# Kernel tuning notes

Hardware: AMD Instinct MI355X
Metric: run time of the kernel (lower is better)

## Reference

```python
import jax, jax.numpy as jnp
import numpy as np

B, SQ, SK, D, H, F = 8, 512, 1024, 1024, 16, 4096
DK = D // H
NEG_INF = -jnp.inf


def _linear(x, w, b):
    return x @ w + b


def _mha(q, k, v, wq, bq, wk, bk, wv, bv, wo, bo, causal, kv_mask):
    # q: [B,Sq,D], k/v: [B,Sk,D]
    b, sq, d = q.shape
    sk = k.shape[1]
    Q = _linear(q, wq, bq).reshape(b, sq, H, DK).transpose(0, 2, 1, 3)  # [B,H,Sq,dk]
    K = _linear(k, wk, bk).reshape(b, sk, H, DK).transpose(0, 2, 1, 3)
    V = _linear(v, wv, bv).reshape(b, sk, H, DK).transpose(0, 2, 1, 3)
    S = jnp.einsum('bhqd,bhkd->bhqk', Q, K) / jnp.sqrt(jnp.asarray(DK, Q.dtype))
    if kv_mask is not None:
        S = jnp.where(kv_mask[:, None, None, :] == 0, NEG_INF, S)
    if causal:
        tri = jnp.tril(jnp.ones((sq, sk), dtype=bool))
        S = jnp.where(tri, S, NEG_INF)
    A = jax.nn.softmax(S, axis=-1)  # dropout p=0 -> identity
    x = jnp.einsum('bhqk,bhkd->bhqd', A, V).transpose(0, 2, 1, 3).reshape(b, sq, d)
    return _linear(x, wo, bo), A


def _ln(x, g, beta, eps=1e-5):
    mu = jnp.mean(x, axis=-1, keepdims=True)
    var = jnp.mean(jnp.square(x - mu), axis=-1, keepdims=True)
    return (x - mu) * jax.lax.rsqrt(var + eps) * g + beta


def setup_inputs() -> dict:
    key = jax.random.key(0)
    ks = jax.random.split(key, 32)
    s = 0.02
    inp = {
        'x': jax.random.normal(ks[0], (B, SQ, D), jnp.float32),
        'enc_o': jax.random.normal(ks[1], (B, SK, D), jnp.float32),
        'enc_mask': jax.random.randint(ks[2], (B, SK), 0, 2, jnp.int32),
    }
    i = 3
    for pfx in ('a1', 'a2'):
        for nm in ('wq', 'wk', 'wv', 'wo'):
            inp[f'{pfx}_{nm}'] = jax.random.normal(ks[i], (D, D), jnp.float32) * s; i += 1
            inp[f'{pfx}_{nm[1:] and "b" + nm[1:]}'] = jnp.zeros((D,), jnp.float32)
    inp['ff_w1'] = jax.random.normal(ks[i], (D, F), jnp.float32) * s; i += 1
    inp['ff_b1'] = jnp.zeros((F,), jnp.float32)
    inp['ff_w2'] = jax.random.normal(ks[i], (F, D), jnp.float32) * s; i += 1
    inp['ff_b2'] = jnp.zeros((D,), jnp.float32)
    for n in ('ln1', 'ln2', 'ln3'):
        inp[f'{n}_g'] = jnp.ones((D,), jnp.float32)
        inp[f'{n}_b'] = jnp.zeros((D,), jnp.float32)
    return inp


def reference(x, enc_o, enc_mask,
              a1_wq, a1_bq, a1_wk, a1_bk, a1_wv, a1_bv, a1_wo, a1_bo,
              a2_wq, a2_bq, a2_wk, a2_bk, a2_wv, a2_bv, a2_wo, a2_bo,
              ff_w1, ff_b1, ff_w2, ff_b2,
              ln1_g, ln1_b, ln2_g, ln2_b, ln3_g, ln3_b):
    res, _ = _mha(x, x, x, a1_wq, a1_bq, a1_wk, a1_bk, a1_wv, a1_bv, a1_wo, a1_bo,
                  causal=True, kv_mask=None)
    x = _ln(x + res, ln1_g, ln1_b)
    res, attn = _mha(x, enc_o, enc_o, a2_wq, a2_bq, a2_wk, a2_bk, a2_wv, a2_bv, a2_wo, a2_bo,
                     causal=False, kv_mask=enc_mask)
    x = _ln(x + res, ln2_g, ln2_b)
    res = _linear(jax.nn.relu(_linear(x, ff_w1, ff_b1)), ff_w2, ff_b2)
    x = _ln(x + res, ln3_g, ln3_b)
    return (x, attn)
```

## Files before the change

kernel.cpp:

```cpp
#include <hip/hip_runtime.h>
#include <hip/hip_bf16.h>


using bf16 = __hip_bfloat16;
typedef __attribute__((ext_vector_type(8))) short short8;
typedef __attribute__((ext_vector_type(4))) float f32x4;

#define DEVINL __device__ __forceinline__

DEVINL unsigned short bf16bits(float f) {
  __hip_bfloat16 h = __float2bfloat16(f);
  return *reinterpret_cast<unsigned short*>(&h);
}
DEVINL float bits2f(unsigned short u) {
  return __uint_as_float(((unsigned int)u) << 16);
}
DEVINL float tofloat(float f) { return f; }
DEVINL float tofloat(bf16 h) { return __bfloat162float(h); }

#define GLD16(gp, lp) __builtin_amdgcn_global_load_lds( \
    (__attribute__((address_space(1))) const void*)(gp), \
    (__attribute__((address_space(3))) void*)(lp), 16, 0, 0)

struct GemmP {
  const bf16* A; const bf16* Bt; void* C;
  const float* bias; const int* kmask;
  float scale;
  int M, N, K, lda, ldb, ldc;
  long sAb, sAh, sBb, sBh, sCb, sCh;
};

enum { EPI_BIAS_BF16 = 0, EPI_CAUSAL_BF16, EPI_KMASK_F32, EPI_NONE_BF16,
       EPI_BIAS_F32, EPI_BIAS_RELU_BF16, EPI_PART_F32 };

template<int EPI>
__global__ __launch_bounds__(256)
void gemm_k(GemmP p) {
  __shared__ bf16 As[128 * 32];
  __shared__ bf16 Bs[128 * 32];
  const int t = threadIdx.x;
  const int lane = t & 63;
  const int w = t >> 6;
  const int z = blockIdx.z;
  const int zb = z >> 4, zh = z & 15;
  const int m0 = blockIdx.y * 128, n0 = blockIdx.x * 128;

  const bf16* Ab = p.A + (long)zb * p.sAb + (long)zh * p.sAh;
  const bf16* Bb = p.Bt + (long)zb * p.sBb + (long)zh * p.sBh;
  const int fl = lane & 15, fq = lane >> 4;
  const int wm = (w >> 1) * 64, wn = (w & 1) * 64;

  f32x4 acc[4][4];
#pragma unroll
  for (int i = 0; i < 4; ++i)
#pragma unroll
    for (int j = 0; j < 4; ++j) acc[i][j] = (f32x4){0.f, 0.f, 0.f, 0.f};

  const int sr = t >> 2;
  const int sc = (t & 3) * 8;
  char* ldsA = (char*)As + w * 1024;
  char* ldsB = (char*)Bs + w * 1024;

  int brow0 = n0 + sr;      if (brow0 > p.N - 1) brow0 = p.N - 1;
  int brow1 = n0 + sr + 64; if (brow1 > p.N - 1) brow1 = p.N - 1;

  for (int k0 = 0; k0 < p.K; k0 += 32) {
    GLD16(Ab + (long)(m0 + sr) * p.lda + k0 + sc, ldsA);
    GLD16(Ab + (long)(m0 + sr + 64) * p.lda + k0 + sc, ldsA + 4096);
    GLD16(Bb + (long)brow0 * p.ldb + k0 + sc, ldsB);
    GLD16(Bb + (long)brow1 * p.ldb + k0 + sc, ldsB + 4096);
    __syncthreads();

    short8 af[4], bfv[4];
#pragma unroll
    for (int i = 0; i < 4; ++i)
      af[i] = *(const short8*)(As + (wm + i * 16 + fl) * 32 + fq * 8);
#pragma unroll
    for (int j = 0; j < 4; ++j)
      bfv[j] = *(const short8*)(Bs + (wn + j * 16 + fl) * 32 + fq * 8);
#pragma unroll
    for (int i = 0; i < 4; ++i)
#pragma unroll
      for (int j = 0; j < 4; ++j)
        acc[i][j] = __builtin_amdgcn_mfma_f32_16x16x32_bf16(af[i], bfv[j], acc[i][j], 0, 0, 0);
    __syncthreads();
  }

  const float NEGINF = -__builtin_inff();
  const long cbase = (long)zb * p.sCb + (long)zh * p.sCh;
#pragma unroll
  for (int i = 0; i < 4; ++i) {
#pragma unroll
    for (int j = 0; j < 4; ++j) {
#pragma unroll
      for (int r = 0; r < 4; ++r) {
        int row = m0 + wm + i * 16 + fq * 4 + r;
        int col = n0 + wn + j * 16 + fl;
        if (col < p.N) {
          float v = acc[i][j][r];
          if (EPI == EPI_BIAS_BF16 || EPI == EPI_BIAS_F32 || EPI == EPI_BIAS_RELU_BF16)
            v += p.bias[col];
          if (EPI == EPI_BIAS_RELU_BF16) v = v > 0.f ? v : 0.f;
          if (EPI == EPI_CAUSAL_BF16) { v *= p.scale; if (col > row) v = NEGINF; }
          if (EPI == EPI_KMASK_F32)   { v *= p.scale; if (p.kmask[zb * 1024 + col] == 0) v = NEGINF; }
          long off = cbase + (long)row * p.ldc + col;
          if (EPI == EPI_KMASK_F32 || EPI == EPI_BIAS_F32 || EPI == EPI_PART_F32)
            ((float*)p.C)[off] = v;
          else ((bf16*)p.C)[off] = __float2bfloat16(v);
        }
      }
    }
  }
}

struct AttnP {
  const bf16 *Q, *K, *Vt;
  float* Pout; bf16* O;
  const int* kmask;
  int ldq, ldk, ldv;
  long sQb, sQh, sKb, sKh, sVb, sVh, sPb, sPh, sOb, sOh;
};

template<int SK, bool CAUSAL, bool WRITE_P>
__global__ __launch_bounds__(512)
void attn_fused_k(AttnP p) {
  constexpr int TKMAX = SK / 64;
  __shared__ bf16 S[64 * SK];
  __shared__ bf16 ring[3 * 4096];
  const int t = threadIdx.x;
  const int lane = t & 63;
  const int w = t >> 6;
  const int fl = lane & 15, fq = lane >> 4;
  const int qh = w >> 2;
  const int wc = w & 3;
  const int zb = blockIdx.z >> 4, zh = blockIdx.z & 15;
  const int q0 = blockIdx.y * 64;
  const float NEGINF = -__builtin_inff();

  const bf16* Qb = p.Q + (long)zb * p.sQb + (long)zh * p.sQh;
  const bf16* Kb = p.K + (long)zb * p.sKb + (long)zh * p.sKh;
  const bf16* Vb = p.Vt + (long)zb * p.sVb + (long)zh * p.sVh;

  const int Tk = CAUSAL ? (q0 >> 6) + 1 : TKMAX;

  short8 af[2][2];
#pragma unroll
  for (int i = 0; i < 2; ++i)
#pragma unroll
    for (int kk = 0; kk < 2; ++kk)
      af[i][kk] = *(const short8*)(Qb + (long)(q0 + qh * 32 + i * 16 + fl) * p.ldq + kk * 32 + fq * 8);

  int kmv[CAUSAL ? 1 : TKMAX];
  if (!CAUSAL) {
#pragma unroll
    for (int kt = 0; kt < TKMAX; ++kt)
      kmv[kt] = p.kmask[zb * 1024 + kt * 64 + wc * 16 + fl];
  }

  const int so = t * 16;
  const int srow = so >> 7;
  const int scb = (so & 127) ^ ((srow & 7) << 4);
  auto stage = [&](const bf16* mb, int ld, int roff, int coff, int buf) {
    GLD16(mb + (long)(roff + srow) * ld + coff + (scb >> 1),
          (char*)ring + buf * 8192 + so);
  };

  stage(Kb, p.ldk, 0, 0, 0);
  if (Tk > 1) stage(Kb, p.ldk, 64, 0, 1);
  for (int kt = 0; kt < Tk; ++kt) {
    if (kt + 1 < Tk) asm volatile("s_waitcnt vmcnt(1)" ::: "memory");
    else             asm volatile("s_waitcnt vmcnt(0)" ::: "memory");
    __builtin_amdgcn_s_barrier();
    if (kt + 2 < Tk) stage(Kb, p.ldk, (kt + 2) * 64, 0, (kt + 2) % 3);

    const char* kb = (const char*)ring + (kt % 3) * 8192;
    const int krow = wc * 16 + fl;
    short8 bfv[2];
#pragma unroll
    for (int kk = 0; kk < 2; ++kk)
      bfv[kk] = *(const short8*)(kb + ((krow * 128 + kk * 64 + fq * 16) ^ ((krow & 7) << 4)));
    f32x4 acc[2] = {(f32x4){0.f,0.f,0.f,0.f}, (f32x4){0.f,0.f,0.f,0.f}};
#pragma unroll
    for (int kk = 0; kk < 2; ++kk) {
      acc[0] = __builtin_amdgcn_mfma_f32_16x16x32_bf16(af[0][kk], bfv[kk], acc[0], 0, 0, 0);
      acc[1] = __builtin_amdgcn_mfma_f32_16x16x32_bf16(af[1][kk], bfv[kk], acc[1], 0, 0, 0);
    }
    const int col = kt * 64 + wc * 16 + fl;
    const bool mok = CAUSAL || (kmv[CAUSAL ? 0 : kt] != 0);
#pragma unroll
    for (int i = 0; i < 2; ++i) {
#pragma unroll
      for (int r = 0; r < 4; ++r) {
        int row = qh * 32 + i * 16 + fq * 4 + r;
        float v = acc[i][r] * 0.125f;
        if (CAUSAL) { if (col > q0 + row) v = NEGINF; }
        else if (!mok) v = NEGINF;
        int b = ((row * SK + col) * 2) ^ ((row & 7) << 4);
        *(bf16*)((char*)S + b) = __float2bfloat16(v);
      }
    }
  }
  asm volatile("s_waitcnt lgkmcnt(0)" ::: "memory");
  __builtin_amdgcn_s_barrier();

  const int Tv = Tk;
  stage(Vb, p.ldv, 0, 0, 0);
  if (Tv > 1) stage(Vb, p.ldv, 0, 64, 1);

  float* Pf = WRITE_P ? (p.Pout + (long)zb * p.sPb + (long)zh * p.sPh) : nullptr;
  constexpr int NC = SK / 512;
  const int lim = Tk * 64;
  for (int rr = 0; rr < 8; ++rr) {
    const int row = w * 8 + rr;
    const int swz = (row & 7) << 4;
    float fv[NC][8];
#pragma unroll
    for (int c = 0; c < NC; ++c) {
      const int col = c * 512 + lane * 8;
      if (!CAUSAL || col < lim) {
        short8 sv = *(const short8*)((char*)S + (((row * SK + col) * 2) ^ swz));
#pragma unroll
        for (int j = 0; j < 8; ++j) fv[c][j] = bits2f((unsigned short)sv[j]);
      } else {
#pragma unroll
        for (int j = 0; j < 8; ++j) fv[c][j] = NEGINF;
      }
    }
    float mx = fv[0][0];
#pragma unroll
    for (int c = 0; c < NC; ++c)
#pragma unroll
      for (int j = 0; j < 8; ++j) mx = fmaxf(mx, fv[c][j]);
    for (int off = 32; off; off >>= 1) mx = fmaxf(mx, __shfl_xor(mx, off, 64));
    float s = 0.f;
#pragma unroll
    for (int c = 0; c < NC; ++c)
#pragma unroll
      for (int j = 0; j < 8; ++j) { fv[c][j] = expf(fv[c][j] - mx); s += fv[c][j]; }
    for (int off = 32; off; off >>= 1) s += __shfl_xor(s, off, 64);
    const float inv = 1.f / s;
#pragma unroll
    for (int c = 0; c < NC; ++c) {
      const int col = c * 512 + lane * 8;
      if (!CAUSAL || col < lim) {
        short8 o;
#pragma unroll
        for (int j = 0; j < 8; ++j) o[j] = (short)bf16bits(fv[c][j] * inv);
        *(short8*)((char*)S + (((row * SK + col) * 2) ^ swz)) = o;
        if (WRITE_P) {
          float* pp = Pf + (long)(q0 + row) * SK + col;
          f32x4 o0, o1;
#pragma unroll
          for (int j = 0; j < 4; ++j) { o0[j] = fv[c][j] * inv; o1[j] = fv[c][4 + j] * inv; }
          *(f32x4*)pp = o0;
          *(f32x4*)(pp + 4) = o1;
        }
      }
    }
  }
  asm volatile("s_waitcnt lgkmcnt(0)" ::: "memory");
  __builtin_amdgcn_s_barrier();

  f32x4 ao[2] = {(f32x4){0.f,0.f,0.f,0.f}, (f32x4){0.f,0.f,0.f,0.f}};
  for (int vt = 0; vt < Tv; ++vt) {
    if (vt + 1 < Tv) asm volatile("s_waitcnt vmcnt(1)" ::: "memory");
    else             asm volatile("s_waitcnt vmcnt(0)" ::: "memory");
    __builtin_amdgcn_s_barrier();
    if (vt + 2 < Tv) stage(Vb, p.ldv, 0, (vt + 2) * 64, (vt + 2) % 3);

    const char* vbuf = (const char*)ring + (vt % 3) * 8192;
    const int vrow = wc * 16 + fl;
    short8 bv[2];
#pragma unroll
    for (int kk = 0; kk < 2; ++kk)
      bv[kk] = *(const short8*)(vbuf + ((vrow * 128 + kk * 64 + fq * 16) ^ ((vrow & 7) << 4)));
#pragma unroll
    for (int i = 0; i < 2; ++i) {
      const int row = qh * 32 + i * 16 + fl;
#pragma unroll
      for (int kk = 0; kk < 2; ++kk) {
        const int col = vt * 64 + kk * 32 + fq * 8;
        short8 pa = *(const short8*)((char*)S + (((row * SK + col) * 2) ^ ((row & 7) << 4)));
        ao[i] = __builtin_amdgcn_mfma_f32_16x16x32_bf16(pa, bv[kk], ao[i], 0, 0, 0);
      }
    }
  }

  bf16* Ob_ = p.O + (long)zb * p.sOb + (long)zh * p.sOh;
#pragma unroll
  for (int i = 0; i < 2; ++i)
#pragma unroll
    for (int r = 0; r < 4; ++r) {
      int row = q0 + qh * 32 + i * 16 + fq * 4 + r;
      Ob_[(long)row * 1024 + wc * 16 + fl] = __float2bfloat16(ao[i][r]);
    }
}

__global__ __launch_bounds__(256)
void ln_k(const float* __restrict__ x, const float* __restrict__ r,
          const float* __restrict__ g, const float* __restrict__ bt,
          float* __restrict__ outf, bf16* __restrict__ outb) {
  const int lane = threadIdx.x & 63;
  const long row = (long)blockIdx.x * 4 + (threadIdx.x >> 6);
  const float* px = x + row * 1024;
  const float* pr = r + row * 1024;
  float4 v[4];
  float s = 0.f;
#pragma unroll
  for (int c = 0; c < 4; ++c) {
    float4 a = *(const float4*)(px + c * 256 + lane * 4);
    float4 b = *(const float4*)(pr + c * 256 + lane * 4);
    v[c].x = a.x + b.x; v[c].y = a.y + b.y; v[c].z = a.z + b.z; v[c].w = a.w + b.w;
    s += v[c].x + v[c].y + v[c].z + v[c].w;
  }
  for (int off = 32; off; off >>= 1) s += __shfl_xor(s, off, 64);
  float mu = s * (1.f / 1024.f);
  float q = 0.f;
#pragma unroll
  for (int c = 0; c < 4; ++c) {
    float dx = v[c].x - mu, dy = v[c].y - mu, dz = v[c].z - mu, dw = v[c].w - mu;
    q += dx * dx + dy * dy + dz * dz + dw * dw;
  }
  for (int off = 32; off; off >>= 1) q += __shfl_xor(q, off, 64);
  float rs = rsqrtf(q * (1.f / 1024.f) + 1e-5f);
#pragma unroll
  for (int c = 0; c < 4; ++c) {
    int col = c * 256 + lane * 4;
    float4 gg = *(const float4*)(g + col);
    float4 bb = *(const float4*)(bt + col);
    float4 o;
    o.x = (v[c].x - mu) * rs * gg.x + bb.x;
    o.y = (v[c].y - mu) * rs * gg.y + bb.y;
    o.z = (v[c].z - mu) * rs * gg.z + bb.z;
    o.w = (v[c].w - mu) * rs * gg.w + bb.w;
    *(float4*)(outf + row * 1024 + col) = o;
    if (outb) {
      uint2 pk;
      pk.x = bf16bits(o.x) | ((unsigned)bf16bits(o.y) << 16);
      pk.y = bf16bits(o.z) | ((unsigned)bf16bits(o.w) << 16);
      *(uint2*)(outb + row * 1024 + col) = pk;
    }
  }
}

template<typename TI>
__global__ __launch_bounds__(256)
void transpose_k(const TI* __restrict__ in, bf16* __restrict__ out,
                 int R, int C, int ldi, int ldo,
                 long sInb, long sInh, long sOutb, long sOuth) {
  __shared__ float tile[32][33];
  const int zb = blockIdx.z >> 4, zh = blockIdx.z & 15;
  const TI* pin = in + (long)zb * sInb + (long)zh * sInh;
  bf16* pout = out + (long)zb * sOutb + (long)zh * sOuth;
  const int c0 = blockIdx.x * 32, r0 = blockIdx.y * 32;
  const int tx = threadIdx.x & 31, ty = threadIdx.x >> 5;
#pragma unroll
  for (int i = 0; i < 32; i += 8)
    tile[ty + i][tx] = tofloat(pin[(long)(r0 + ty + i) * ldi + c0 + tx]);
  __syncthreads();
#pragma unroll
  for (int i = 0; i < 32; i += 8)
    pout[(long)(c0 + ty + i) * ldo + r0 + tx] = __float2bfloat16(tile[tx][ty + i]);
}

__global__ __launch_bounds__(256) void cvt_k(const float* __restrict__ in,
                                             bf16* __restrict__ out, long n4) {
  long i = (long)blockIdx.x * 256 + threadIdx.x;
  if (i < n4) {
    float4 v = *(const float4*)(in + i * 4);
    uint2 pk;
    pk.x = bf16bits(v.x) | ((unsigned)bf16bits(v.y) << 16);
    pk.y = bf16bits(v.z) | ((unsigned)bf16bits(v.w) << 16);
    *(uint2*)(out + i * 4) = pk;
  }
}

__global__ __launch_bounds__(256)
void concatb_k(float* dst, const float* a, const float* b, const float* c,
               int n, int total) {
  int i = blockIdx.x * 256 + threadIdx.x;
  if (i >= total) return;
  float v = (i < n) ? a[i] : (i < 2 * n ? b[i - n] : c[i - 2 * n]);
  dst[i] = v;
}

__global__ __launch_bounds__(256)
void reduce4_k(const float* __restrict__ part, const float* __restrict__ bias,
               float* __restrict__ out) {
  long i = ((long)blockIdx.x * 256 + threadIdx.x) * 4;
  float4 a = *(const float4*)(part + i);
  float4 b = *(const float4*)(part + 4194304 + i);
  float4 c = *(const float4*)(part + 2 * 4194304 + i);
  float4 d = *(const float4*)(part + 3 * 4194304 + i);
  float4 bi = *(const float4*)(bias + (int)(i & 1023));
  float4 o;
  o.x = a.x + b.x + c.x + d.x + bi.x;
  o.y = a.y + b.y + c.y + d.y + bi.y;
  o.z = a.z + b.z + c.z + d.z + bi.z;
  o.w = a.w + b.w + c.w + d.w + bi.w;
  *(float4*)(out + i) = o;
}

static inline GemmP mkp(const void* A, const bf16* Bt, void* C,
                        const float* bias, const int* km, float sc,
                        int M, int N, int K, int lda, int ldb, int ldc,
                        long sAb, long sAh, long sBb, long sBh, long sCb, long sCh) {
  GemmP p;
  p.A = (const bf16*)A; p.Bt = Bt; p.C = C; p.bias = bias; p.kmask = km; p.scale = sc;
  p.M = M; p.N = N; p.K = K; p.lda = lda; p.ldb = ldb; p.ldc = ldc;
  p.sAb = sAb; p.sAh = sAh; p.sBb = sBb; p.sBh = sBh; p.sCb = sCb; p.sCh = sCh;
  return p;
}

extern "C" void kernel_launch(void* const* d_in, const int* in_sizes, int n_in,
                              void* d_out, int out_size, void* d_ws, size_t ws_size,
                              hipStream_t stream) {
  const float* x        = (const float*)d_in[0];
  const float* enc_o    = (const float*)d_in[1];
  const int*   enc_mask = (const int*)d_in[2];
  const float* a1_wq = (const float*)d_in[3];  const float* a1_bq = (const float*)d_in[4];
  const float* a1_wk = (const float*)d_in[5];  const float* a1_bk = (const float*)d_in[6];
  const float* a1_wv = (const float*)d_in[7];  const float* a1_bv = (const float*)d_in[8];
  const float* a1_wo = (const float*)d_in[9];  const float* a1_bo = (const float*)d_in[10];
  const float* a2_wq = (const float*)d_in[11]; const float* a2_bq = (const float*)d_in[12];
  const float* a2_wk = (const float*)d_in[13]; const float* a2_bk = (const float*)d_in[14];
  const float* a2_wv = (const float*)d_in[15]; const float* a2_bv = (const float*)d_in[16];
  const float* a2_wo = (const float*)d_in[17]; const float* a2_bo = (const float*)d_in[18];
  const float* ff_w1 = (const float*)d_in[19]; const float* ff_b1 = (const float*)d_in[20];
  const float* ff_w2 = (const float*)d_in[21]; const float* ff_b2 = (const float*)d_in[22];
  const float* ln1_g = (const float*)d_in[23]; const float* ln1_b = (const float*)d_in[24];
  const float* ln2_g = (const float*)d_in[25]; const float* ln2_b = (const float*)d_in[26];
  const float* ln3_g = (const float*)d_in[27]; const float* ln3_b = (const float*)d_in[28];

  const size_t MB = 1u << 20;
  const long M1 = 1048576;
  char* w = (char*)d_ws;
  bf16*  xb   = (bf16*)(w + 0);
  bf16*  encb = (bf16*)(w + 8 * MB);
  float* x1f  = (float*)(w + 24 * MB);
  float* x2f  = (float*)(w + 40 * MB);
  bf16*  xcb  = (bf16*)(w + 56 * MB);
  bf16*  wT   = (bf16*)(w + 64 * MB);
  float* bqkv = (float*)(w + 96 * MB);
  float* bkv  = (float*)(w + 96 * MB + 16384);
  bf16*  QKV  = (bf16*)(w + 104 * MB);
  bf16*  KVc  = (bf16*)(w + 128 * MB);
  bf16*  Vt   = (bf16*)(w + 160 * MB);
  bf16*  Ob   = (bf16*)(w + 176 * MB);
  float* res  = (float*)(w + 184 * MB);
  float* part = (float*)(w + 200 * MB);
  bf16*  Asf  = (bf16*)(w + 264 * MB);

  float* out_x = (float*)d_out;
  float* attn  = (float*)d_out + 4194304;

  const dim3 blk(256);
  const dim3 blk5(512);

  cvt_k<<<4096, blk, 0, stream>>>(x, xb, 1048576);
  cvt_k<<<8192, blk, 0, stream>>>(enc_o, encb, 2097152);
  {
    dim3 tg(32, 32, 1);
    transpose_k<float><<<tg, blk, 0, stream>>>(a1_wq, wT + 0 * M1, 1024, 1024, 1024, 1024, 0,0,0,0);
    transpose_k<float><<<tg, blk, 0, stream>>>(a1_wk, wT + 1 * M1, 1024, 1024, 1024, 1024, 0,0,0,0);
    transpose_k<float><<<tg, blk, 0, stream>>>(a1_wv, wT + 2 * M1, 1024, 1024, 1024, 1024, 0,0,0,0);
    transpose_k<float><<<tg, blk, 0, stream>>>(a1_wo, wT + 3 * M1, 1024, 1024, 1024, 1024, 0,0,0,0);
    transpose_k<float><<<tg, blk, 0, stream>>>(a2_wq, wT + 4 * M1, 1024, 1024, 1024, 1024, 0,0,0,0);
    transpose_k<float><<<tg, blk, 0, stream>>>(a2_wk, wT + 5 * M1, 1024, 1024, 1024, 1024, 0,0,0,0);
    transpose_k<float><<<tg, blk, 0, stream>>>(a2_wv, wT + 6 * M1, 1024, 1024, 1024, 1024, 0,0,0,0);
    transpose_k<float><<<tg, blk, 0, stream>>>(a2_wo, wT + 7 * M1, 1024, 1024, 1024, 1024, 0,0,0,0);
    transpose_k<float><<<dim3(128, 32, 1), blk, 0, stream>>>(ff_w1, wT + 8 * M1, 1024, 4096, 4096, 1024, 0,0,0,0);
    transpose_k<float><<<dim3(32, 128, 1), blk, 0, stream>>>(ff_w2, wT + 12 * M1, 4096, 1024, 1024, 4096, 0,0,0,0);
  }
  concatb_k<<<12, blk, 0, stream>>>(bqkv, a1_bq, a1_bk, a1_bv, 1024, 3072);
  concatb_k<<<8, blk, 0, stream>>>(bkv, a2_bk, a2_bv, a2_bv, 1024, 2048);

  gemm_k<EPI_BIAS_BF16><<<dim3(24, 32, 1), blk, 0, stream>>>(
      mkp(xb, wT, QKV, bqkv, nullptr, 0.f, 4096, 3072, 1024, 1024, 1024, 3072, 0,0,0,0,0,0));
  bf16* Qs = QKV;
  bf16* Ks = QKV + 1024;
  bf16* Vs = QKV + 2048;

  transpose_k<bf16><<<dim3(2, 16, 128), blk, 0, stream>>>(
      Vs, Vt, 512, 64, 3072, 512, 1572864, 64, 524288, 32768);

  {
    AttnP ap;
    ap.Q = Qs; ap.K = Ks; ap.Vt = Vt; ap.Pout = nullptr; ap.O = Ob; ap.kmask = nullptr;
    ap.ldq = 3072; ap.ldk = 3072; ap.ldv = 512;
    ap.sQb = 1572864; ap.sQh = 64; ap.sKb = 1572864; ap.sKh = 64;
    ap.sVb = 524288;  ap.sVh = 32768; ap.sPb = 0; ap.sPh = 0;
    ap.sOb = 524288;  ap.sOh = 64;
    attn_fused_k<512, true, false><<<dim3(1, 8, 128), blk5, 0, stream>>>(ap);
  }

  gemm_k<EPI_BIAS_F32><<<dim3(8, 32, 1), blk, 0, stream>>>(
      mkp(Ob, wT + 3 * M1, res, a1_bo, nullptr, 0.f, 4096, 1024, 1024, 1024, 1024, 1024, 0,0,0,0,0,0));

  ln_k<<<1024, blk, 0, stream>>>(x, res, ln1_g, ln1_b, x1f, xcb);

  gemm_k<EPI_BIAS_BF16><<<dim3(8, 32, 1), blk, 0, stream>>>(
      mkp(xcb, wT + 4 * M1, QKV, a2_bq, nullptr, 0.f, 4096, 1024, 1024, 1024, 1024, 1024, 0,0,0,0,0,0));
  gemm_k<EPI_BIAS_BF16><<<dim3(16, 64, 1), blk, 0, stream>>>(
      mkp(encb, wT + 5 * M1, KVc, bkv, nullptr, 0.f, 8192, 2048, 1024, 1024, 1024, 2048, 0,0,0,0,0,0));
  bf16* Qc = QKV;
  bf16* Kc = KVc;
  bf16* Vc = KVc + 1024;

  transpose_k<bf16><<<dim3(2, 32, 128), blk, 0, stream>>>(
      Vc, Vt, 1024, 64, 2048, 1024, 2097152, 64, 1048576, 65536);

  {
    AttnP ap;
    ap.Q = Qc; ap.K = Kc; ap.Vt = Vt; ap.Pout = attn; ap.O = Ob; ap.kmask = enc_mask;
    ap.ldq = 1024; ap.ldk = 2048; ap.ldv = 1024;
    ap.sQb = 524288;  ap.sQh = 64; ap.sKb = 2097152; ap.sKh = 64;
    ap.sVb = 1048576; ap.sVh = 65536; ap.sPb = 8388608; ap.sPh = 524288;
    ap.sOb = 524288;  ap.sOh = 64;
    attn_fused_k<1024, false, true><<<dim3(1, 8, 128), blk5, 0, stream>>>(ap);
  }

  gemm_k<EPI_BIAS_F32><<<dim3(8, 32, 1), blk, 0, stream>>>(
      mkp(Ob, wT + 7 * M1, res, a2_bo, nullptr, 0.f, 4096, 1024, 1024, 1024, 1024, 1024, 0,0,0,0,0,0));

  ln_k<<<1024, blk, 0, stream>>>(x1f, res, ln2_g, ln2_b, x2f, xcb);

  gemm_k<EPI_BIAS_RELU_BF16><<<dim3(32, 32, 1), blk, 0, stream>>>(
      mkp(xcb, wT + 8 * M1, Asf, ff_b1, nullptr, 0.f, 4096, 4096, 1024, 1024, 1024, 4096, 0,0,0,0,0,0));
  gemm_k<EPI_PART_F32><<<dim3(8, 32, 4), blk, 0, stream>>>(
      mkp(Asf, wT + 12 * M1, part, nullptr, nullptr, 0.f, 4096, 1024, 1024, 4096, 4096, 1024,
          0, 1024, 0, 1024, 0, 4194304));
  reduce4_k<<<4096, blk, 0, stream>>>(part, ff_b2, res);

  ln_k<<<1024, blk, 0, stream>>>(x2f, res, ln3_g, ln3_b, out_x, nullptr);
}
```

Baseline: 1.044 ms.

## Merge prep kernels, batch projection GEMMs, split-K out-proj with LN-fused reduction

```diff
diff --git a/kernel.cpp b/kernel.cpp
--- a/kernel.cpp
+++ b/kernel.cpp
@@ -34,16 +34,14 @@
        EPI_BIAS_F32, EPI_BIAS_RELU_BF16, EPI_PART_F32 };
 
 template<int EPI>
-__global__ __launch_bounds__(256)
-void gemm_k(GemmP p) {
+DEVINL void gemm_body(const GemmP& p, int bx, int by, int bz) {
   __shared__ bf16 As[128 * 32];
   __shared__ bf16 Bs[128 * 32];
   const int t = threadIdx.x;
   const int lane = t & 63;
   const int w = t >> 6;
-  const int z = blockIdx.z;
-  const int zb = z >> 4, zh = z & 15;
-  const int m0 = blockIdx.y * 128, n0 = blockIdx.x * 128;
+  const int zb = bz >> 4, zh = bz & 15;
+  const int m0 = by * 128, n0 = bx * 128;
 
   const bf16* Ab = p.A + (long)zb * p.sAb + (long)zh * p.sAh;
   const bf16* Bb = p.Bt + (long)zb * p.sBb + (long)zh * p.sBh;
@@ -113,6 +111,20 @@
   }
 }
 
+template<int EPI>
+__global__ __launch_bounds__(256)
+void gemm_k(GemmP p) {
+  gemm_body<EPI>(p, blockIdx.x, blockIdx.y, blockIdx.z);
+}
+
+struct Gemm2P { GemmP a, b; int nA, axw, bxw; };
+__global__ __launch_bounds__(256)
+void gemm2_k(Gemm2P q) {
+  const int b = blockIdx.x;
+  if (b < q.nA) gemm_body<EPI_BIAS_BF16>(q.a, b % q.axw, b / q.axw, 0);
+  else { const int c = b - q.nA; gemm_body<EPI_BIAS_BF16>(q.b, c % q.bxw, c / q.bxw, 0); }
+}
+
 struct AttnP {
   const bf16 *Q, *K, *Vt;
   float* Pout; bf16* O;
@@ -296,21 +308,28 @@
     }
 }
 
+template<int NP>
 __global__ __launch_bounds__(256)
-void ln_k(const float* __restrict__ x, const float* __restrict__ r,
-          const float* __restrict__ g, const float* __restrict__ bt,
-          float* __restrict__ outf, bf16* __restrict__ outb) {
+void ln_fuse_k(const float* __restrict__ x, const float* __restrict__ part, long pstride,
+               const float* __restrict__ pb,
+               const float* __restrict__ g, const float* __restrict__ bt,
+               float* __restrict__ outf, bf16* __restrict__ outb) {
   const int lane = threadIdx.x & 63;
   const long row = (long)blockIdx.x * 4 + (threadIdx.x >> 6);
   const float* px = x + row * 1024;
-  const float* pr = r + row * 1024;
   float4 v[4];
   float s = 0.f;
 #pragma unroll
   for (int c = 0; c < 4; ++c) {
-    float4 a = *(const float4*)(px + c * 256 + lane * 4);
-    float4 b = *(const float4*)(pr + c * 256 + lane * 4);
-    v[c].x = a.x + b.x; v[c].y = a.y + b.y; v[c].z = a.z + b.z; v[c].w = a.w + b.w;
+    const int col = c * 256 + lane * 4;
+    float4 a = *(const float4*)(px + col);
+    float4 bb = *(const float4*)(pb + col);
+    v[c].x = a.x + bb.x; v[c].y = a.y + bb.y; v[c].z = a.z + bb.z; v[c].w = a.w + bb.w;
+#pragma unroll
+    for (int sl = 0; sl < NP; ++sl) {
+      float4 pp = *(const float4*)(part + sl * pstride + row * 1024 + col);
+      v[c].x += pp.x; v[c].y += pp.y; v[c].z += pp.z; v[c].w += pp.w;
+    }
     s += v[c].x + v[c].y + v[c].z + v[c].w;
   }
   for (int off = 32; off; off >>= 1) s += __shfl_xor(s, off, 64);
@@ -344,16 +363,9 @@
 }
 
 template<typename TI>
-__global__ __launch_bounds__(256)
-void transpose_k(const TI* __restrict__ in, bf16* __restrict__ out,
-                 int R, int C, int ldi, int ldo,
-                 long sInb, long sInh, long sOutb, long sOuth) {
-  __shared__ float tile[32][33];
-  const int zb = blockIdx.z >> 4, zh = blockIdx.z & 15;
-  const TI* pin = in + (long)zb * sInb + (long)zh * sInh;
-  bf16* pout = out + (long)zb * sOutb + (long)zh * sOuth;
-  const int c0 = blockIdx.x * 32, r0 = blockIdx.y * 32;
-  const int tx = threadIdx.x & 31, ty = threadIdx.x >> 5;
+DEVINL void tr_body(const TI* __restrict__ pin, bf16* __restrict__ pout,
+                    int ldi, int ldo, int c0, int r0, int t, float tile[32][33]) {
+  const int tx = t & 31, ty = t >> 5;
 #pragma unroll
   for (int i = 0; i < 32; i += 8)
     tile[ty + i][tx] = tofloat(pin[(long)(r0 + ty + i) * ldi + c0 + tx]);
@@ -363,42 +375,66 @@
     pout[(long)(c0 + ty + i) * ldo + r0 + tx] = __float2bfloat16(tile[tx][ty + i]);
 }
 
-__global__ __launch_bounds__(256) void cvt_k(const float* __restrict__ in,
-                                             bf16* __restrict__ out, long n4) {
-  long i = (long)blockIdx.x * 256 + threadIdx.x;
-  if (i < n4) {
-    float4 v = *(const float4*)(in + i * 4);
+struct PrepP {
+  const float *x, *enc;
+  const float* wsrc[10];
+  const float *b0, *b1, *b2, *b4, *b5;
+  bf16 *xb, *encb, *wT;
+  float *bqkv, *bkv;
+};
+__global__ __launch_bounds__(256)
+void prep_k(PrepP p) {
+  __shared__ float tile[32][33];
+  const int b = blockIdx.x, t = threadIdx.x;
+  if (b < 12288) {
+    const float* src = (b < 4096) ? p.x : p.enc;
+    bf16* dst = (b < 4096) ? p.xb : p.encb;
+    long i = (long)(b < 4096 ? b : b - 4096) * 256 + t;
+    float4 v = *(const float4*)(src + i * 4);
     uint2 pk;
     pk.x = bf16bits(v.x) | ((unsigned)bf16bits(v.y) << 16);
     pk.y = bf16bits(v.z) | ((unsigned)bf16bits(v.w) << 16);
-    *(uint2*)(out + i * 4) = pk;
-  }
-}
-
+    *(uint2*)(dst + i * 4) = pk;
+  } else if (b < 20480) {
+    int l = b - 12288; int wdx = l >> 10; l &= 1023;
+    tr_body<float>(p.wsrc[wdx], p.wT + (long)wdx * 1048576, 1024, 1024,
+                   (l & 31) * 32, (l >> 5) * 32, t, tile);
+  } else if (b < 24576) {
+    int l = b - 20480;
+    tr_body<float>(p.wsrc[8], p.wT + 8l * 1048576, 4096, 1024,
+                   (l & 127) * 32, (l >> 7) * 32, t, tile);
+  } else if (b < 28672) {
+    int l = b - 24576;
+    tr_body<float>(p.wsrc[9], p.wT + 12l * 1048576, 1024, 4096,
+                   (l % 32) * 32, (l / 32) * 32, t, tile);
+  } else if (b < 28684) {
+    int i = (b - 28672) * 256 + t;
+    p.bqkv[i] = (i < 1024) ? p.b0[i] : (i < 2048 ? p.b1[i - 1024] : p.b2[i - 2048]);
+  } else {
+    int i = (b - 28684) * 256 + t;
+    p.bkv[i] = (i < 1024) ? p.b4[i] : p.b5[i - 1024];
+  }
+}
+
+struct Vt2P { const bf16 *vs, *vc; bf16 *vts, *vtc; };
 __global__ __launch_bounds__(256)
-void concatb_k(float* dst, const float* a, const float* b, const float* c,
-               int n, int total) {
-  int i = blockIdx.x * 256 + threadIdx.x;
-  if (i >= total) return;
-  float v = (i < n) ? a[i] : (i < 2 * n ? b[i - n] : c[i - 2 * n]);
-  dst[i] = v;
-}
-
-__global__ __launch_bounds__(256)
-void reduce4_k(const float* __restrict__ part, const float* __restrict__ bias,
-               float* __restrict__ out) {
-  long i = ((long)blockIdx.x * 256 + threadIdx.x) * 4;
-  float4 a = *(const float4*)(part + i);
-  float4 b = *(const float4*)(part + 4194304 + i);
-  float4 c = *(const float4*)(part + 2 * 4194304 + i);
-  float4 d = *(const float4*)(part + 3 * 4194304 + i);
-  float4 bi = *(const float4*)(bias + (int)(i & 1023));
-  float4 o;
-  o.x = a.x + b.x + c.x + d.x + bi.x;
-  o.y = a.y + b.y + c.y + d.y + bi.y;
-  o.z = a.z + b.z + c.z + d.z + bi.z;
-  o.w = a.w + b.w + c.w + d.w + bi.w;
-  *(float4*)(out + i) = o;
+void vt2_k(Vt2P p) {
+  __shared__ float tile[32][33];
+  const int b = blockIdx.x, t = threadIdx.x;
+  if (b < 4096) {
+    int z = b >> 5, l = b & 31;
+    int zb = z >> 4, zh = z & 15;
+    tr_body<bf16>(p.vs + (long)zb * 1572864 + zh * 64,
+                  p.vts + (long)zb * 524288 + zh * 32768,
+                  3072, 512, (l & 1) * 32, (l >> 1) * 32, t, tile);
+  } else {
+    int c = b - 4096;
+    int z = c >> 6, l = c & 63;
+    int zb = z >> 4, zh = z & 15;
+    tr_body<bf16>(p.vc + (long)zb * 2097152 + zh * 64,
+                  p.vtc + (long)zb * 1048576 + zh * 65536,
+                  2048, 1024, (l & 1) * 32, (l >> 1) * 32, t, tile);
+  }
 }
 
 static inline GemmP mkp(const void* A, const bf16* Bt, void* C,
@@ -445,11 +481,11 @@
   float* bkv  = (float*)(w + 96 * MB + 16384);
   bf16*  QKV  = (bf16*)(w + 104 * MB);
   bf16*  KVc  = (bf16*)(w + 128 * MB);
-  bf16*  Vt   = (bf16*)(w + 160 * MB);
+  bf16*  VtS  = (bf16*)(w + 160 * MB);
   bf16*  Ob   = (bf16*)(w + 176 * MB);
-  float* res  = (float*)(w + 184 * MB);
   float* part = (float*)(w + 200 * MB);
   bf16*  Asf  = (bf16*)(w + 264 * MB);
+  bf16*  VtC  = (bf16*)(w + 332 * MB);
 
   float* out_x = (float*)d_out;
   float* attn  = (float*)d_out + 4194304;
@@ -457,36 +493,38 @@
   const dim3 blk(256);
   const dim3 blk5(512);
 
-  cvt_k<<<4096, blk, 0, stream>>>(x, xb, 1048576);
-  cvt_k<<<8192, blk, 0, stream>>>(enc_o, encb, 2097152);
   {
-    dim3 tg(32, 32, 1);
-    transpose_k<float><<<tg, blk, 0, stream>>>(a1_wq, wT + 0 * M1, 1024, 1024, 1024, 1024, 0,0,0,0);
-    transpose_k<float><<<tg, blk, 0, stream>>>(a1_wk, wT + 1 * M1, 1024, 1024, 1024, 1024, 0,0,0,0);
-    transpose_k<float><<<tg, blk, 0, stream>>>(a1_wv, wT + 2 * M1, 1024, 1024, 1024, 1024, 0,0,0,0);
-    transpose_k<float><<<tg, blk, 0, stream>>>(a1_wo, wT + 3 * M1, 1024, 1024, 1024, 1024, 0,0,0,0);
-    transpose_k<float><<<tg, blk, 0, stream>>>(a2_wq, wT + 4 * M1, 1024, 1024, 1024, 1024, 0,0,0,0);
-    transpose_k<float><<<tg, blk, 0, stream>>>(a2_wk, wT + 5 * M1, 1024, 1024, 1024, 1024, 0,0,0,0);
-    transpose_k<float><<<tg, blk, 0, stream>>>(a2_wv, wT + 6 * M1, 1024, 1024, 1024, 1024, 0,0,0,0);
-    transpose_k<float><<<tg, blk, 0, stream>>>(a2_wo, wT + 7 * M1, 1024, 1024, 1024, 1024, 0,0,0,0);
-    transpose_k<float><<<dim3(128, 32, 1), blk, 0, stream>>>(ff_w1, wT + 8 * M1, 1024, 4096, 4096, 1024, 0,0,0,0);
-    transpose_k<float><<<dim3(32, 128, 1), blk, 0, stream>>>(ff_w2, wT + 12 * M1, 4096, 1024, 1024, 4096, 0,0,0,0);
-  }
-  concatb_k<<<12, blk, 0, stream>>>(bqkv, a1_bq, a1_bk, a1_bv, 1024, 3072);
-  concatb_k<<<8, blk, 0, stream>>>(bkv, a2_bk, a2_bv, a2_bv, 1024, 2048);
-
-  gemm_k<EPI_BIAS_BF16><<<dim3(24, 32, 1), blk, 0, stream>>>(
-      mkp(xb, wT, QKV, bqkv, nullptr, 0.f, 4096, 3072, 1024, 1024, 1024, 3072, 0,0,0,0,0,0));
+    PrepP pp;
+    pp.x = x; pp.enc = enc_o;
+    pp.wsrc[0] = a1_wq; pp.wsrc[1] = a1_wk; pp.wsrc[2] = a1_wv; pp.wsrc[3] = a1_wo;
+    pp.wsrc[4] = a2_wq; pp.wsrc[5] = a2_wk; pp.wsrc[6] = a2_wv; pp.wsrc[7] = a2_wo;
+    pp.wsrc[8] = ff_w1; pp.wsrc[9] = ff_w2;
+    pp.b0 = a1_bq; pp.b1 = a1_bk; pp.b2 = a1_bv; pp.b4 = a2_bk; pp.b5 = a2_bv;
+    pp.xb = xb; pp.encb = encb; pp.wT = wT; pp.bqkv = bqkv; pp.bkv = bkv;
+    prep_k<<<28692, blk, 0, stream>>>(pp);
+  }
+
+  {
+    Gemm2P q;
+    q.a = mkp(xb, wT, QKV, bqkv, nullptr, 0.f, 4096, 3072, 1024, 1024, 1024, 3072, 0,0,0,0,0,0);
+    q.b = mkp(encb, wT + 5 * M1, KVc, bkv, nullptr, 0.f, 8192, 2048, 1024, 1024, 1024, 2048, 0,0,0,0,0,0);
+    q.nA = 768; q.axw = 24; q.bxw = 16;
+    gemm2_k<<<1792, blk, 0, stream>>>(q);
+  }
   bf16* Qs = QKV;
   bf16* Ks = QKV + 1024;
   bf16* Vs = QKV + 2048;
-
-  transpose_k<bf16><<<dim3(2, 16, 128), blk, 0, stream>>>(
-      Vs, Vt, 512, 64, 3072, 512, 1572864, 64, 524288, 32768);
+  bf16* Kc = KVc;
+  bf16* Vc = KVc + 1024;
+
+  {
+    Vt2P vp; vp.vs = Vs; vp.vc = Vc; vp.vts = VtS; vp.vtc = VtC;
+    vt2_k<<<12288, blk, 0, stream>>>(vp);
+  }
 
   {
     AttnP ap;
-    ap.Q = Qs; ap.K = Ks; ap.Vt = Vt; ap.Pout = nullptr; ap.O = Ob; ap.kmask = nullptr;
+    ap.Q = Qs; ap.K = Ks; ap.Vt = VtS; ap.Pout = nullptr; ap.O = Ob; ap.kmask = nullptr;
     ap.ldq = 3072; ap.ldk = 3072; ap.ldv = 512;
     ap.sQb = 1572864; ap.sQh = 64; ap.sKb = 1572864; ap.sKh = 64;
     ap.sVb = 524288;  ap.sVh = 32768; ap.sPb = 0; ap.sPh = 0;
@@ -494,25 +532,19 @@
     attn_fused_k<512, true, false><<<dim3(1, 8, 128), blk5, 0, stream>>>(ap);
   }
 
-  gemm_k<EPI_BIAS_F32><<<dim3(8, 32, 1), blk, 0, stream>>>(
-      mkp(Ob, wT + 3 * M1, res, a1_bo, nullptr, 0.f, 4096, 1024, 1024, 1024, 1024, 1024, 0,0,0,0,0,0));
-
-  ln_k<<<1024, blk, 0, stream>>>(x, res, ln1_g, ln1_b, x1f, xcb);
+  gemm_k<EPI_PART_F32><<<dim3(8, 32, 2), blk, 0, stream>>>(
+      mkp(Ob, wT + 3 * M1, part, nullptr, nullptr, 0.f, 4096, 1024, 512, 1024, 1024, 1024,
+          0, 512, 0, 512, 0, 4194304));
+
+  ln_fuse_k<2><<<1024, blk, 0, stream>>>(x, part, 4194304, a1_bo, ln1_g, ln1_b, x1f, xcb);
 
   gemm_k<EPI_BIAS_BF16><<<dim3(8, 32, 1), blk, 0, stream>>>(
       mkp(xcb, wT + 4 * M1, QKV, a2_bq, nullptr, 0.f, 4096, 1024, 1024, 1024, 1024, 1024, 0,0,0,0,0,0));
-  gemm_k<EPI_BIAS_BF16><<<dim3(16, 64, 1), blk, 0, stream>>>(
-      mkp(encb, wT + 5 * M1, KVc, bkv, nullptr, 0.f, 8192, 2048, 1024, 1024, 1024, 2048, 0,0,0,0,0,0));
   bf16* Qc = QKV;
-  bf16* Kc = KVc;
-  bf16* Vc = KVc + 1024;
-
-  transpose_k<bf16><<<dim3(2, 32, 128), blk, 0, stream>>>(
-      Vc, Vt, 1024, 64, 2048, 1024, 2097152, 64, 1048576, 65536);
 
   {
     AttnP ap;
-    ap.Q = Qc; ap.K = Kc; ap.Vt = Vt; ap.Pout = attn; ap.O = Ob; ap.kmask = enc_mask;
+    ap.Q = Qc; ap.K = Kc; ap.Vt = VtC; ap.Pout = attn; ap.O = Ob; ap.kmask = enc_mask;
     ap.ldq = 1024; ap.ldk = 2048; ap.ldv = 1024;
     ap.sQb = 524288;  ap.sQh = 64; ap.sKb = 2097152; ap.sKh = 64;
     ap.sVb = 1048576; ap.sVh = 65536; ap.sPb = 8388608; ap.sPh = 524288;
@@ -520,17 +552,18 @@
     attn_fused_k<1024, false, true><<<dim3(1, 8, 128), blk5, 0, stream>>>(ap);
   }
 
-  gemm_k<EPI_BIAS_F32><<<dim3(8, 32, 1), blk, 0, stream>>>(
-      mkp(Ob, wT + 7 * M1, res, a2_bo, nullptr, 0.f, 4096, 1024, 1024, 1024, 1024, 1024, 0,0,0,0,0,0));
-
-  ln_k<<<1024, blk, 0, stream>>>(x1f, res, ln2_g, ln2_b, x2f, xcb);
+  gemm_k<EPI_PART_F32><<<dim3(8, 32, 2), blk, 0, stream>>>(
+      mkp(Ob, wT + 7 * M1, part, nullptr, nullptr, 0.f, 4096, 1024, 512, 1024, 1024, 1024,
+          0, 512, 0, 512, 0, 4194304));
+
+  ln_fuse_k<2><<<1024, blk, 0, stream>>>(x1f, part, 4194304, a2_bo, ln2_g, ln2_b, x2f, xcb);
 
   gemm_k<EPI_BIAS_RELU_BF16><<<dim3(32, 32, 1), blk, 0, stream>>>(
       mkp(xcb, wT + 8 * M1, Asf, ff_b1, nullptr, 0.f, 4096, 4096, 1024, 1024, 1024, 4096, 0,0,0,0,0,0));
+
   gemm_k<EPI_PART_F32><<<dim3(8, 32, 4), blk, 0, stream>>>(
       mkp(Asf, wT + 12 * M1, part, nullptr, nullptr, 0.f, 4096, 1024, 1024, 4096, 4096, 1024,
           0, 1024, 0, 1024, 0, 4194304));
-  reduce4_k<<<4096, blk, 0, stream>>>(part, ff_b2, res);
-
-  ln_k<<<1024, blk, 0, stream>>>(x2f, res, ln3_g, ln3_b, out_x, nullptr);
-}
+
+  ln_fuse_k<4><<<1024, blk, 0, stream>>>(x2f, part, 4194304, ff_b2, ln3_g, ln3_b, out_x, nullptr);
+}
```

Result: faster. 988.8 us (-5.3%).
